# Kernel optimization log

Measured on AMD Instinct MI355X. Metric: run time of the kernel, lower is better.

The kernel has to match this reference:

```python
import jax, jax.numpy as jnp
import numpy as np

N = 12000       # num nodes
E = 384000      # num edges (avg degree 32)
F_IN = 512      # num_feats
H = 64          # gnn_hid_dim (== anchor_dim)
C = 7           # num_cls
SIGMA = 1.0


def setup_inputs() -> dict:
    key = jax.random.key(0)
    ks = jax.random.split(key, 9)
    scale = lambda fan_in: 1.0 / np.sqrt(fan_in)
    return {
        "x": jax.random.normal(ks[0], (N, F_IN), dtype=jnp.float32),
        "W1": jax.random.normal(ks[1], (F_IN, H), dtype=jnp.float32) * scale(F_IN),
        "b1": jnp.zeros((H,), dtype=jnp.float32),
        "W2": jax.random.normal(ks[2], (H, H), dtype=jnp.float32) * scale(H),
        "b2": jnp.zeros((H,), dtype=jnp.float32),
        "aux": jax.random.normal(ks[3], (H,), dtype=jnp.float32),
        "clf_W": jax.random.normal(ks[4], (2 * H, C), dtype=jnp.float32) * scale(2 * H),
        "clf_b": jnp.zeros((C,), dtype=jnp.float32),
        "edge_index": jax.random.randint(ks[5], (2, E), 0, N, dtype=jnp.int64),
    }


def gcn_conv(x, W, b, src, dst, n):
    # GCNConv: D^{-1/2} (A + I) D^{-1/2} X W + b, with self-loops
    h = x @ W                                                   # [N, out]
    deg = jax.ops.segment_sum(jnp.ones(src.shape[0], h.dtype), dst,
                              num_segments=n) + 1.0             # +1 for self-loop
    inv_sqrt = jax.lax.rsqrt(deg)
    norm = inv_sqrt[src] * inv_sqrt[dst]                        # [E]
    agg = jax.ops.segment_sum(h[src] * norm[:, None], dst, num_segments=n)
    agg = agg + h / deg[:, None]                                # self-loop term (norm = 1/deg)
    return agg + b


def reference(x, W1, b1, W2, b2, aux, clf_W, clf_b, edge_index):
    src, dst = edge_index[0], edge_index[1]
    n = x.shape[0]
    h = jax.nn.relu(gcn_conv(x, W1, b1, src, dst, n))
    h = gcn_conv(h, W2, b2, src, dst, n)                        # [N, H]
    # kernel aggregate: pairwise Gaussian kernel on cosine scores
    a = aux / jnp.maximum(jnp.linalg.norm(aux), 1e-12)          # F.normalize
    hn = jnp.maximum(jnp.linalg.norm(h, axis=-1), 1e-8)         # cosine_similarity eps
    score = (h @ a) / hn                                        # [N]
    diff = score[None, :] - score[:, None]                      # [N, N]
    kappa = jnp.exp(-(diff * diff) / (SIGMA * SIGMA))           # [N, N]
    z = (kappa @ h) / jnp.sum(kappa, axis=1, keepdims=True)     # [N, H]
    return jnp.concatenate([h, z], axis=-1) @ clf_W + clf_b     # [N, C]
```

## Files before the change

kernel.cpp:

```cpp
#include <hip/hip_runtime.h>
#include <hip/hip_bf16.h>

#define N_NODES 12000
#define N_EDGES 384000
#define F_IN 512
#define H 64
#define C_CLS 7
#define KTERMS 16
#define PAD 96
#define CSTR 32
#define MOM_BLKS 96
#define NB 4

__device__ __forceinline__ float wred_f(float x) {
    #pragma unroll
    for (int o = 32; o > 0; o >>= 1) x += __shfl_xor(x, o);
    return x;
}

__global__ __launch_bounds__(256) void k1_gemm_fill(const float* __restrict__ x,
                                                    const float* __restrict__ W1,
                                                    const int* __restrict__ ei,
                                                    float* __restrict__ hbuf,
                                                    int* __restrict__ cur,
                                                    int* __restrict__ csrc) {
    const int b = blockIdx.x, t = threadIdx.x;
    if (b < 750) {
        __shared__ float xsT[64 * 19];
        __shared__ float wsm[64 * 64];
        const int tx = t & 15, ty = t >> 4;
        const int i0 = b * 16;
        float acc[4] = {};
        for (int k0 = 0; k0 < F_IN; k0 += 64) {
            {
                float4 v = *(const float4*)(x + (size_t)(i0 + ty) * F_IN + k0 + tx * 4);
                xsT[(tx * 4 + 0) * 19 + ty] = v.x;
                xsT[(tx * 4 + 1) * 19 + ty] = v.y;
                xsT[(tx * 4 + 2) * 19 + ty] = v.z;
                xsT[(tx * 4 + 3) * 19 + ty] = v.w;
            }
            #pragma unroll
            for (int q = 0; q < 4; ++q) {
                int idx = t + q * 256;
                int r = idx >> 4, c4 = idx & 15;
                *(float4*)(&wsm[r * 64 + c4 * 4]) =
                    *(const float4*)(W1 + (size_t)(k0 + r) * H + c4 * 4);
            }
            __syncthreads();
            #pragma unroll
            for (int kk = 0; kk < 64; ++kk) {
                float a = xsT[kk * 19 + ty];
                float4 bb = *(const float4*)(&wsm[kk * 64 + tx * 4]);
                acc[0] += a * bb.x; acc[1] += a * bb.y;
                acc[2] += a * bb.z; acc[3] += a * bb.w;
            }
            __syncthreads();
        }
        *(float4*)(hbuf + (size_t)(i0 + ty) * H + tx * 4) =
            make_float4(acc[0], acc[1], acc[2], acc[3]);
    } else {
        for (int e = (b - 750) * 256 + t; e < N_EDGES; e += 250 * 256) {
            int s = ei[e];
            int d = ei[N_EDGES + e];
            int pos = atomicAdd(&cur[d * CSTR], 1);
            if (pos < PAD) csrc[d * PAD + pos] = s;
        }
    }
}

__global__ __launch_bounds__(256) void invs_k(const int* __restrict__ cur,
                                              float* __restrict__ invs) {
    int i = blockIdx.x * 256 + threadIdx.x;
    if (i < N_NODES) invs[i] = rsqrtf((float)cur[i * CSTR] + 1.0f);
}

__global__ __launch_bounds__(256) void agg1_k(const float* __restrict__ hbuf,
                                              const float* __restrict__ b1,
                                              const int* __restrict__ cur,
                                              const int* __restrict__ csrc,
                                              const float* __restrict__ invs,
                                              float* __restrict__ h1) {
    __shared__ int2 sPair[NB * PAD];
    __shared__ int sDeg[NB];
    __shared__ float sIsd[NB];
    const int t = threadIdx.x, f = t & 63, w = t >> 6;
    const int base = blockIdx.x * NB;
    if (t < NB) {
        sDeg[t] = min(cur[(base + t) * CSTR], PAD);
        sIsd[t] = invs[base + t];
    }
    __syncthreads();
    for (int idx = t; idx < NB * PAD; idx += 256) {
        int n = idx / PAD, e = idx - n * PAD;
        if (e < sDeg[n]) {
            int s = csrc[(base + n) * PAD + e];
            sPair[idx] = make_int2(s, __float_as_int(invs[s]));
        }
    }
    __syncthreads();
    const int i = base + w;
    const int deg = sDeg[w];
    const float isd = sIsd[w];
    const int2* pp = sPair + w * PAD;
    float acc = 0.f;
    int e = 0;
    for (; e + 4 <= deg; e += 4) {
        int2 p0 = pp[e], p1 = pp[e + 1], p2 = pp[e + 2], p3 = pp[e + 3];
        acc += hbuf[p0.x * H + f] * __int_as_float(p0.y)
             + hbuf[p1.x * H + f] * __int_as_float(p1.y)
             + hbuf[p2.x * H + f] * __int_as_float(p2.y)
             + hbuf[p3.x * H + f] * __int_as_float(p3.y);
    }
    for (; e < deg; ++e) {
        int2 p = pp[e];
        acc += hbuf[p.x * H + f] * __int_as_float(p.y);
    }
    float res = (acc + hbuf[i * H + f] * isd) * isd + b1[f];
    h1[i * H + f] = fmaxf(res, 0.f);
}

__global__ __launch_bounds__(256) void agg2_k(const float* __restrict__ h1,
                                              const float* __restrict__ W2,
                                              const float* __restrict__ b2,
                                              const float* __restrict__ aux,
                                              const int* __restrict__ cur,
                                              const int* __restrict__ csrc,
                                              const float* __restrict__ invs,
                                              float* __restrict__ h2,
                                              float* __restrict__ score) {
    __shared__ float w2s[64 * 64];
    __shared__ int2 sPair[NB * PAD];
    __shared__ int sDeg[NB];
    __shared__ float sIsd[NB];
    __shared__ float anorm[64];
    __shared__ float gsh[NB * 64];
    const int t = threadIdx.x, f = t & 63, w = t >> 6;
    const int base = blockIdx.x * NB;
    #pragma unroll
    for (int q = 0; q < 4; ++q) {
        int idx = t + q * 256;
        int r = idx >> 4, c4 = idx & 15;
        *(float4*)(&w2s[r * 64 + c4 * 4]) = *(const float4*)(W2 + r * H + c4 * 4);
    }
    if (t < NB) {
        sDeg[t] = min(cur[(base + t) * CSTR], PAD);
        sIsd[t] = invs[base + t];
    }
    if (t < 64) {
        float av = aux[t];
        anorm[t] = av * rsqrtf(fmaxf(wred_f(av * av), 1e-24f));
    }
    __syncthreads();
    for (int idx = t; idx < NB * PAD; idx += 256) {
        int n = idx / PAD, e = idx - n * PAD;
        if (e < sDeg[n]) {
            int s = csrc[(base + n) * PAD + e];
            sPair[idx] = make_int2(s, __float_as_int(invs[s]));
        }
    }
    __syncthreads();
    const int i = base + w;
    const int deg = sDeg[w];
    const float isd = sIsd[w];
    const int2* pp = sPair + w * PAD;
    float acc = 0.f;
    int e = 0;
    for (; e + 4 <= deg; e += 4) {
        int2 p0 = pp[e], p1 = pp[e + 1], p2 = pp[e + 2], p3 = pp[e + 3];
        acc += h1[p0.x * H + f] * __int_as_float(p0.y)
             + h1[p1.x * H + f] * __int_as_float(p1.y)
             + h1[p2.x * H + f] * __int_as_float(p2.y)
             + h1[p3.x * H + f] * __int_as_float(p3.y);
    }
    for (; e < deg; ++e) {
        int2 p = pp[e];
        acc += h1[p.x * H + f] * __int_as_float(p.y);
    }
    float g = (acc + h1[i * H + f] * isd) * isd;
    gsh[w * 64 + f] = g;
    __builtin_amdgcn_wave_barrier();
    float hv = b2[f];
    #pragma unroll 16
    for (int k = 0; k < 64; ++k) hv += gsh[w * 64 + k] * w2s[k * 64 + f];
    h2[i * H + f] = hv;
    float dp = wred_f(hv * anorm[f]);
    float nn = wred_f(hv * hv);
    if (f == 0) score[i] = dp / fmaxf(sqrtf(nn), 1e-8f);
}

__global__ __launch_bounds__(256) void momden_k(const float* __restrict__ h2,
                                                const float* __restrict__ score,
                                                double* __restrict__ M,
                                                double* __restrict__ m0) {
    const int t = threadIdx.x, f = t & 63, g = t >> 6;
    float accM[KTERMS], accD[KTERMS];
    #pragma unroll
    for (int k = 0; k < KTERMS; ++k) { accM[k] = 0.f; accD[k] = 0.f; }
    for (int j = blockIdx.x * 4 + g; j < N_NODES; j += MOM_BLKS * 4) {
        float sj = score[j];
        float wj = expf(-sj * sj);
        float hv = h2[j * H + f];
        float tm = wj * hv, td = wj;
        #pragma unroll
        for (int k = 0; k < KTERMS; ++k) {
            accM[k] += tm; tm *= sj;
            accD[k] += td; td *= sj;
        }
    }
    __shared__ float Msh[4 * KTERMS * 64];
    __shared__ float Dsh[4 * KTERMS];
    #pragma unroll
    for (int k = 0; k < KTERMS; ++k) Msh[(g * KTERMS + k) * 64 + f] = accM[k];
    if (f == 0) {
        #pragma unroll
        for (int k = 0; k < KTERMS; ++k) Dsh[g * KTERMS + k] = accD[k];
    }
    __syncthreads();
    for (int idx = t; idx < KTERMS * 64; idx += 256) {
        int k = idx >> 6, ff = idx & 63;
        float sum = Msh[(0 * KTERMS + k) * 64 + ff] + Msh[(1 * KTERMS + k) * 64 + ff]
                  + Msh[(2 * KTERMS + k) * 64 + ff] + Msh[(3 * KTERMS + k) * 64 + ff];
        unsafeAtomicAdd(&M[idx], (double)sum);
    }
    if (t < KTERMS) {
        float sum = Dsh[t] + Dsh[KTERMS + t] + Dsh[2 * KTERMS + t] + Dsh[3 * KTERMS + t];
        unsafeAtomicAdd(&m0[t], (double)sum);
    }
}

__global__ __launch_bounds__(256) void final_k(const float* __restrict__ h2,
                                               const float* __restrict__ score,
                                               const double* __restrict__ M,
                                               const double* __restrict__ m0,
                                               const float* __restrict__ clfW,
                                               const float* __restrict__ clfb,
                                               float* __restrict__ out) {
    __shared__ float Ms[KTERMS * 64];
    __shared__ float m0s[KTERMS];
    __shared__ float cw[128 * C_CLS];
    __shared__ float cb[8];
    __shared__ float zh[4 * 128];
    const int t = threadIdx.x, f = t & 63, w = t >> 6;
    for (int idx = t; idx < KTERMS * 64; idx += 256) Ms[idx] = (float)M[idx];
    if (t < KTERMS) m0s[t] = (float)m0[t];
    for (int idx = t; idx < 128 * C_CLS; idx += 256) cw[idx] = clfW[idx];
    if (t < C_CLS) cb[t] = clfb[t];
    __syncthreads();
    const int base = blockIdx.x * 16;
    for (int q = 0; q < 4; ++q) {
        int i = base + q * 4 + w;
        float s = score[i];
        float c = expf(-s * s);
        float t2 = 2.f * s;
        float num = 0.f, den = 0.f;
        #pragma unroll
        for (int k = 0; k < KTERMS; ++k) {
            num += c * Ms[k * 64 + f];
            den += c * m0s[k];
            c *= t2 * (1.0f / (float)(k + 1));
        }
        zh[w * 128 + f] = h2[i * H + f];
        zh[w * 128 + 64 + f] = num / den;
        __builtin_amdgcn_wave_barrier();
        if (f < C_CLS) {
            float o = cb[f];
            #pragma unroll 8
            for (int u = 0; u < 128; ++u) o += zh[w * 128 + u] * cw[u * C_CLS + f];
            out[(size_t)i * C_CLS + f] = o;
        }
        __builtin_amdgcn_wave_barrier();
    }
}

extern "C" void kernel_launch(void* const* d_in, const int* in_sizes, int n_in,
                              void* d_out, int out_size, void* d_ws, size_t ws_size,
                              hipStream_t stream) {
    (void)in_sizes; (void)n_in; (void)out_size; (void)ws_size;
    const float* x    = (const float*)d_in[0];
    const float* W1   = (const float*)d_in[1];
    const float* b1   = (const float*)d_in[2];
    const float* W2   = (const float*)d_in[3];
    const float* b2   = (const float*)d_in[4];
    const float* aux  = (const float*)d_in[5];
    const float* clfW = (const float*)d_in[6];
    const float* clfb = (const float*)d_in[7];
    const int*   ei   = (const int*)d_in[8];
    float* out = (float*)d_out;
    char* ws = (char*)d_ws;

    float*  hbuf  = (float*)(ws + 0);
    float*  h1    = (float*)(ws + 3072000);
    float*  h2    = (float*)(ws + 6144000);
    float*  score = (float*)(ws + 9216000);
    float*  invs  = (float*)(ws + 9264000);
    int*    csrc  = (int*)  (ws + 9312000);
    int*    cur   = (int*)  (ws + 13920000);
    double* M     = (double*)(ws + 15456000);
    double* m0    = (double*)(ws + 15464192);
    const size_t zero_off = 13920000, zero_sz = 1536000 + 8192 + 128;

    hipMemsetAsync(ws + zero_off, 0, zero_sz, stream);
    k1_gemm_fill<<<1000, 256, 0, stream>>>(x, W1, ei, hbuf, cur, csrc);
    invs_k<<<47, 256, 0, stream>>>(cur, invs);
    agg1_k<<<N_NODES / NB, 256, 0, stream>>>(hbuf, b1, cur, csrc, invs, h1);
    agg2_k<<<N_NODES / NB, 256, 0, stream>>>(h1, W2, b2, aux, cur, csrc, invs, h2, score);
    momden_k<<<MOM_BLKS, 256, 0, stream>>>(h2, score, M, m0);
    final_k<<<750, 256, 0, stream>>>(h2, score, M, m0, clfW, clfb, out);
}
```

Baseline: 98.47 us.

## Retile first GEMM to two rows per thread, add sparse memset kernel, unroll gathers

```diff
diff --git a/kernel.cpp b/kernel.cpp
--- a/kernel.cpp
+++ b/kernel.cpp
@@ -9,13 +9,25 @@
 #define KTERMS 16
 #define PAD 96
 #define CSTR 32
-#define MOM_BLKS 96
+#define MOM_BLKS 192
 #define NB 4
+#define GEMM_BLKS 375
+#define FILL_BLKS 256
+#define XS_STR 68
 
 __device__ __forceinline__ float wred_f(float x) {
     #pragma unroll
     for (int o = 32; o > 0; o >>= 1) x += __shfl_xor(x, o);
     return x;
+}
+
+__global__ __launch_bounds__(256) void init_k(int* __restrict__ cur,
+                                              double* __restrict__ M,
+                                              double* __restrict__ m0) {
+    int i = blockIdx.x * 256 + threadIdx.x;
+    if (i < N_NODES) cur[i * CSTR] = 0;
+    if (i < KTERMS * 64) M[i] = 0.0;
+    if (i < KTERMS) m0[i] = 0.0;
 }
 
 __global__ __launch_bounds__(256) void k1_gemm_fill(const float* __restrict__ x,
@@ -25,41 +37,55 @@
                                                     int* __restrict__ cur,
                                                     int* __restrict__ csrc) {
     const int b = blockIdx.x, t = threadIdx.x;
-    if (b < 750) {
-        __shared__ float xsT[64 * 19];
+    if (b < GEMM_BLKS) {
+        __shared__ float xs[32 * XS_STR];
         __shared__ float wsm[64 * 64];
         const int tx = t & 15, ty = t >> 4;
-        const int i0 = b * 16;
-        float acc[4] = {};
+        const int i0 = b * 32;
+        float acc[2][4] = {};
         for (int k0 = 0; k0 < F_IN; k0 += 64) {
-            {
-                float4 v = *(const float4*)(x + (size_t)(i0 + ty) * F_IN + k0 + tx * 4);
-                xsT[(tx * 4 + 0) * 19 + ty] = v.x;
-                xsT[(tx * 4 + 1) * 19 + ty] = v.y;
-                xsT[(tx * 4 + 2) * 19 + ty] = v.z;
-                xsT[(tx * 4 + 3) * 19 + ty] = v.w;
+            #pragma unroll
+            for (int q = 0; q < 2; ++q) {
+                int idx = t + q * 256;
+                int row = idx >> 4, kg = idx & 15;
+                *(float4*)(&xs[row * XS_STR + kg * 4]) =
+                    *(const float4*)(x + (size_t)(i0 + row) * F_IN + k0 + kg * 4);
             }
             #pragma unroll
             for (int q = 0; q < 4; ++q) {
                 int idx = t + q * 256;
-                int r = idx >> 4, c4 = idx & 15;
-                *(float4*)(&wsm[r * 64 + c4 * 4]) =
-                    *(const float4*)(W1 + (size_t)(k0 + r) * H + c4 * 4);
+                int r = idx >> 4, cg = idx & 15;
+                *(float4*)(&wsm[r * 64 + cg * 4]) =
+                    *(const float4*)(W1 + (size_t)(k0 + r) * H + cg * 4);
             }
             __syncthreads();
             #pragma unroll
-            for (int kk = 0; kk < 64; ++kk) {
-                float a = xsT[kk * 19 + ty];
-                float4 bb = *(const float4*)(&wsm[kk * 64 + tx * 4]);
-                acc[0] += a * bb.x; acc[1] += a * bb.y;
-                acc[2] += a * bb.z; acc[3] += a * bb.w;
+            for (int kk0 = 0; kk0 < 64; kk0 += 4) {
+                float4 a0 = *(const float4*)(&xs[(ty * 2 + 0) * XS_STR + kk0]);
+                float4 a1 = *(const float4*)(&xs[(ty * 2 + 1) * XS_STR + kk0]);
+                float4 b0 = *(const float4*)(&wsm[(kk0 + 0) * 64 + tx * 4]);
+                float4 b1v = *(const float4*)(&wsm[(kk0 + 1) * 64 + tx * 4]);
+                float4 b2v = *(const float4*)(&wsm[(kk0 + 2) * 64 + tx * 4]);
+                float4 b3v = *(const float4*)(&wsm[(kk0 + 3) * 64 + tx * 4]);
+                acc[0][0] += a0.x * b0.x;  acc[0][1] += a0.x * b0.y;  acc[0][2] += a0.x * b0.z;  acc[0][3] += a0.x * b0.w;
+                acc[0][0] += a0.y * b1v.x; acc[0][1] += a0.y * b1v.y; acc[0][2] += a0.y * b1v.z; acc[0][3] += a0.y * b1v.w;
+                acc[0][0] += a0.z * b2v.x; acc[0][1] += a0.z * b2v.y; acc[0][2] += a0.z * b2v.z; acc[0][3] += a0.z * b2v.w;
+                acc[0][0] += a0.w * b3v.x; acc[0][1] += a0.w * b3v.y; acc[0][2] += a0.w * b3v.z; acc[0][3] += a0.w * b3v.w;
+                acc[1][0] += a1.x * b0.x;  acc[1][1] += a1.x * b0.y;  acc[1][2] += a1.x * b0.z;  acc[1][3] += a1.x * b0.w;
+                acc[1][0] += a1.y * b1v.x; acc[1][1] += a1.y * b1v.y; acc[1][2] += a1.y * b1v.z; acc[1][3] += a1.y * b1v.w;
+                acc[1][0] += a1.z * b2v.x; acc[1][1] += a1.z * b2v.y; acc[1][2] += a1.z * b2v.z; acc[1][3] += a1.z * b2v.w;
+                acc[1][0] += a1.w * b3v.x; acc[1][1] += a1.w * b3v.y; acc[1][2] += a1.w * b3v.z; acc[1][3] += a1.w * b3v.w;
             }
             __syncthreads();
         }
-        *(float4*)(hbuf + (size_t)(i0 + ty) * H + tx * 4) =
-            make_float4(acc[0], acc[1], acc[2], acc[3]);
+        #pragma unroll
+        for (int r = 0; r < 2; ++r) {
+            int row = i0 + ty * 2 + r;
+            *(float4*)(hbuf + (size_t)row * H + tx * 4) =
+                make_float4(acc[r][0], acc[r][1], acc[r][2], acc[r][3]);
+        }
     } else {
-        for (int e = (b - 750) * 256 + t; e < N_EDGES; e += 250 * 256) {
+        for (int e = (b - GEMM_BLKS) * 256 + t; e < N_EDGES; e += FILL_BLKS * 256) {
             int s = ei[e];
             int d = ei[N_EDGES + e];
             int pos = atomicAdd(&cur[d * CSTR], 1);
@@ -104,8 +130,20 @@
     const int2* pp = sPair + w * PAD;
     float acc = 0.f;
     int e = 0;
+    for (; e + 8 <= deg; e += 8) {
+        int2 p0 = pp[e], p1 = pp[e+1], p2 = pp[e+2], p3 = pp[e+3];
+        int2 p4 = pp[e+4], p5 = pp[e+5], p6 = pp[e+6], p7 = pp[e+7];
+        acc += hbuf[p0.x * H + f] * __int_as_float(p0.y)
+             + hbuf[p1.x * H + f] * __int_as_float(p1.y)
+             + hbuf[p2.x * H + f] * __int_as_float(p2.y)
+             + hbuf[p3.x * H + f] * __int_as_float(p3.y)
+             + hbuf[p4.x * H + f] * __int_as_float(p4.y)
+             + hbuf[p5.x * H + f] * __int_as_float(p5.y)
+             + hbuf[p6.x * H + f] * __int_as_float(p6.y)
+             + hbuf[p7.x * H + f] * __int_as_float(p7.y);
+    }
     for (; e + 4 <= deg; e += 4) {
-        int2 p0 = pp[e], p1 = pp[e + 1], p2 = pp[e + 2], p3 = pp[e + 3];
+        int2 p0 = pp[e], p1 = pp[e+1], p2 = pp[e+2], p3 = pp[e+3];
         acc += hbuf[p0.x * H + f] * __int_as_float(p0.y)
              + hbuf[p1.x * H + f] * __int_as_float(p1.y)
              + hbuf[p2.x * H + f] * __int_as_float(p2.y)
@@ -165,8 +203,20 @@
     const int2* pp = sPair + w * PAD;
     float acc = 0.f;
     int e = 0;
+    for (; e + 8 <= deg; e += 8) {
+        int2 p0 = pp[e], p1 = pp[e+1], p2 = pp[e+2], p3 = pp[e+3];
+        int2 p4 = pp[e+4], p5 = pp[e+5], p6 = pp[e+6], p7 = pp[e+7];
+        acc += h1[p0.x * H + f] * __int_as_float(p0.y)
+             + h1[p1.x * H + f] * __int_as_float(p1.y)
+             + h1[p2.x * H + f] * __int_as_float(p2.y)
+             + h1[p3.x * H + f] * __int_as_float(p3.y)
+             + h1[p4.x * H + f] * __int_as_float(p4.y)
+             + h1[p5.x * H + f] * __int_as_float(p5.y)
+             + h1[p6.x * H + f] * __int_as_float(p6.y)
+             + h1[p7.x * H + f] * __int_as_float(p7.y);
+    }
     for (; e + 4 <= deg; e += 4) {
-        int2 p0 = pp[e], p1 = pp[e + 1], p2 = pp[e + 2], p3 = pp[e + 3];
+        int2 p0 = pp[e], p1 = pp[e+1], p2 = pp[e+2], p3 = pp[e+3];
         acc += h1[p0.x * H + f] * __int_as_float(p0.y)
              + h1[p1.x * H + f] * __int_as_float(p1.y)
              + h1[p2.x * H + f] * __int_as_float(p2.y)
@@ -297,10 +347,9 @@
     int*    cur   = (int*)  (ws + 13920000);
     double* M     = (double*)(ws + 15456000);
     double* m0    = (double*)(ws + 15464192);
-    const size_t zero_off = 13920000, zero_sz = 1536000 + 8192 + 128;
-
-    hipMemsetAsync(ws + zero_off, 0, zero_sz, stream);
-    k1_gemm_fill<<<1000, 256, 0, stream>>>(x, W1, ei, hbuf, cur, csrc);
+
+    init_k<<<47, 256, 0, stream>>>(cur, M, m0);
+    k1_gemm_fill<<<GEMM_BLKS + FILL_BLKS, 256, 0, stream>>>(x, W1, ei, hbuf, cur, csrc);
     invs_k<<<47, 256, 0, stream>>>(cur, invs);
     agg1_k<<<N_NODES / NB, 256, 0, stream>>>(hbuf, b1, cur, csrc, invs, h1);
     agg2_k<<<N_NODES / NB, 256, 0, stream>>>(h1, W2, b2, aux, cur, csrc, invs, h2, score);
```

New measurement: 94.92 us. 3.6% less time.
